# Optimization experiments

Hardware: AMD Instinct MI355X
Metric: run time of the kernel (lower is better)

## Reference

```python
import jax, jax.numpy as jnp
import numpy as np

N, T, D_IN, D_OUT = 131072, 16, 128, 128


def setup_inputs() -> dict:
    key = jax.random.key(0)
    k1, k2, k3, k4 = jax.random.split(key, 4)
    x = jax.random.normal(k1, (N, D_IN), dtype=jnp.float32)
    # sorted type ids, matching HeteroLinear(is_sorted=True)
    type_vec = jnp.sort(jax.random.randint(k2, (N,), 0, T)).astype(jnp.int32)
    # HeteroLinear weight: [num_types, in_channels, out_channels]; out = x @ W[t] + b[t]
    weight = (jax.random.normal(k3, (T, D_IN, D_OUT), dtype=jnp.float32)
              / np.float32(np.sqrt(D_IN)))
    bias = jax.random.normal(k4, (T, D_OUT), dtype=jnp.float32) * 0.01
    return {"x": x, "type_vec": type_vec, "weight": weight, "bias": bias}


def _grouped_matmul(x, weight, type_vec):
    """Segment (grouped) matmul: rows are sorted by type; row i uses weight[type_vec[i]]."""
    try:
        # Native grouped-GEMM primitive (exploits is_sorted=True contiguity).
        group_sizes = jnp.bincount(type_vec, length=weight.shape[0]).astype(jnp.int32)
        return jax.lax.ragged_dot(x, weight, group_sizes)
    except Exception:
        # Fallback: small fixed loop over the T types, masked accumulate.
        out = jnp.zeros((x.shape[0], weight.shape[-1]), dtype=x.dtype)
        for t in range(weight.shape[0]):
            out = out + jnp.where((type_vec == t)[:, None], x @ weight[t], jnp.zeros((), x.dtype))
        return out


def reference(x, type_vec, weight, bias):
    # ToHeteroLinear.fused_forward == HeteroLinear(x, type_vec):
    #   out[i] = x[i] @ weight[type_vec[i]] + bias[type_vec[i]]
    out = _grouped_matmul(x, weight, type_vec)  # [N, D_OUT]
    return out + bias[type_vec]
```

## Files before the change

### kernel.cpp

```cpp
#include <hip/hip_runtime.h>

#define DD 128
#define BM 64
#define CHUNK 2
#define T_TYPES 16

typedef __bf16 bf16x8 __attribute__((ext_vector_type(8)));
typedef float  f32x4  __attribute__((ext_vector_type(4)));

__device__ __forceinline__ void async_copy16(const void* g, void* l) {
    __builtin_amdgcn_global_load_lds(
        (const __attribute__((address_space(1))) unsigned int*)g,
        (__attribute__((address_space(3))) unsigned int*)l, 16, 0, 0);
}

__global__ __launch_bounds__(256) void transpose_w_frag_kernel(
    const float* __restrict__ w, unsigned short* __restrict__ wbf)
{
    __shared__ float lds[DD * 33];
    const int t   = blockIdx.x >> 2;
    const int n0  = (blockIdx.x & 3) * 32;
    const int tid = threadIdx.x;
    const float* wt = w + (size_t)t * DD * DD;

    #pragma unroll
    for (int i = 0; i < 4; ++i) {
        int f = tid + i * 256;
        int k = f >> 3;
        int c = (f & 7) * 4;
        float4 v = *(const float4*)&wt[k * DD + n0 + c];
        lds[k * 33 + c + 0] = v.x;
        lds[k * 33 + c + 1] = v.y;
        lds[k * 33 + c + 2] = v.z;
        lds[k * 33 + c + 3] = v.w;
    }
    __syncthreads();
    #pragma unroll
    for (int i = 0; i < 4; ++i) {
        int g  = tid + i * 256;
        int nl = g >> 5;
        int k4 = (g & 31) * 4;
        int n  = n0 + nl;
        int nt  = n >> 4, n16 = n & 15;
        int kk  = k4 >> 5, q = (k4 >> 3) & 3, jb = k4 & 7;
        int lane = q * 16 + n16;
        size_t ofs = ((((size_t)t * 8 + nt) * 4 + kk) * 64 + lane) * 8 + jb;
        ushort4 o;
        union { __bf16 b; unsigned short u; } cv;
        cv.b = (__bf16)lds[(k4 + 0) * 33 + nl]; o.x = cv.u;
        cv.b = (__bf16)lds[(k4 + 1) * 33 + nl]; o.y = cv.u;
        cv.b = (__bf16)lds[(k4 + 2) * 33 + nl]; o.z = cv.u;
        cv.b = (__bf16)lds[(k4 + 3) * 33 + nl]; o.w = cv.u;
        *(ushort4*)&wbf[ofs] = o;
    }
}

__global__ __launch_bounds__(256, 4) void hetero_main_kernel(
    const float* __restrict__ x,
    const int*   __restrict__ tv,
    const __bf16* __restrict__ wbf,
    const float* __restrict__ bias,
    float*       __restrict__ out)
{
    __shared__ __bf16 Bs[DD * DD];

    const int tid  = threadIdx.x;
    const int wave = tid >> 6;
    const int lane = tid & 63;
    const int q    = lane >> 4;
    const int n16  = lane & 15;
    const int chunk0 = blockIdx.x * (BM * CHUNK);

    int t_res = tv[chunk0];

    {
        const char* gsrc = (const char*)(wbf + (size_t)t_res * DD * DD);
        char* ldst = (char*)Bs;
        const int wofs = wave * 1024 + lane * 16;
        #pragma unroll
        for (int r = 0; r < 8; ++r)
            async_copy16(gsrc + r * 4096 + wofs, ldst + r * 4096 + wave * 1024);
    }

    float bv[8];
    #pragma unroll
    for (int nt = 0; nt < 8; ++nt) bv[nt] = bias[t_res * DD + nt * 16 + n16];

    f32x4 xlo[4], xhi[4];
    {
        const float* base = x + (size_t)(chunk0 + wave * 16 + n16) * DD + q * 8;
        #pragma unroll
        for (int kk = 0; kk < 4; ++kk) {
            xlo[kk] = *(const f32x4*)(base + kk * 32);
            xhi[kk] = *(const f32x4*)(base + kk * 32 + 4);
        }
    }

    __syncthreads();

    #pragma unroll
    for (int tile = 0; tile < CHUNK; ++tile) {
        const int trow0 = chunk0 + tile * BM;
        const int wrow0 = trow0 + wave * 16;

        f32x4 nlo[4], nhi[4];
        if (tile + 1 < CHUNK) {
            const float* base = x + (size_t)(wrow0 + BM + n16) * DD + q * 8;
            #pragma unroll
            for (int kk = 0; kk < 4; ++kk) {
                nlo[kk] = *(const f32x4*)(base + kk * 32);
                nhi[kk] = *(const f32x4*)(base + kk * 32 + 4);
            }
        }

        bf16x8 a[4];
        #pragma unroll
        for (int kk = 0; kk < 4; ++kk) {
            bf16x8 t;
            t[0] = (__bf16)xlo[kk][0]; t[1] = (__bf16)xlo[kk][1];
            t[2] = (__bf16)xlo[kk][2]; t[3] = (__bf16)xlo[kk][3];
            t[4] = (__bf16)xhi[kk][0]; t[5] = (__bf16)xhi[kk][1];
            t[6] = (__bf16)xhi[kk][2]; t[7] = (__bf16)xhi[kk][3];
            a[kk] = t;
        }

        const int tlo = tv[trow0];
        const int thi = tv[trow0 + BM - 1];

        for (int t = tlo; t <= thi; ++t) {
            if (t != t_res) {
                __syncthreads();
                const char* gsrc = (const char*)(wbf + (size_t)t * DD * DD);
                char* ldst = (char*)Bs;
                const int wofs = wave * 1024 + lane * 16;
                #pragma unroll
                for (int r = 0; r < 8; ++r)
                    async_copy16(gsrc + r * 4096 + wofs, ldst + r * 4096 + wave * 1024);
                t_res = t;
                #pragma unroll
                for (int nt = 0; nt < 8; ++nt) bv[nt] = bias[t * DD + nt * 16 + n16];
                __syncthreads();
            }

            f32x4 acc[8];
            #pragma unroll
            for (int nt = 0; nt < 8; ++nt) acc[nt] = (f32x4){0.f, 0.f, 0.f, 0.f};

            #pragma unroll
            for (int nt = 0; nt < 8; ++nt) {
                #pragma unroll
                for (int kk = 0; kk < 4; ++kk) {
                    bf16x8 b = *(const bf16x8*)&Bs[(((nt << 2) | kk) << 9) | (lane << 3)];
                    acc[nt] = __builtin_amdgcn_mfma_f32_16x16x32_bf16(a[kk], b, acc[nt], 0, 0, 0);
                }
            }

            const int rbase = wrow0 + q * 4;
            bool m0 = true, m1 = true, m2 = true, m3 = true;
            if (tlo != thi) {
                m0 = (tv[rbase + 0] == t);
                m1 = (tv[rbase + 1] == t);
                m2 = (tv[rbase + 2] == t);
                m3 = (tv[rbase + 3] == t);
            }
            float* o = out + (size_t)rbase * DD + n16;
            #pragma unroll
            for (int nt = 0; nt < 8; ++nt) {
                float* oc = o + nt * 16;
                if (m0) oc[0 * DD] = acc[nt][0] + bv[nt];
                if (m1) oc[1 * DD] = acc[nt][1] + bv[nt];
                if (m2) oc[2 * DD] = acc[nt][2] + bv[nt];
                if (m3) oc[3 * DD] = acc[nt][3] + bv[nt];
            }
        }

        #pragma unroll
        for (int kk = 0; kk < 4; ++kk) { xlo[kk] = nlo[kk]; xhi[kk] = nhi[kk]; }
    }
}

extern "C" void kernel_launch(void* const* d_in, const int* in_sizes, int n_in,
                              void* d_out, int out_size, void* d_ws, size_t ws_size,
                              hipStream_t stream) {
    const float* x    = (const float*)d_in[0];
    const int*   tv   = (const int*)d_in[1];
    const float* w    = (const float*)d_in[2];
    const float* bias = (const float*)d_in[3];
    float*       out  = (float*)d_out;
    unsigned short* wbf = (unsigned short*)d_ws;

    int nrows = in_sizes[0] / DD;
    int grid  = nrows / (BM * CHUNK);

    hipLaunchKernelGGL(transpose_w_frag_kernel, dim3(T_TYPES * 4), dim3(256), 0, stream,
                       w, wbf);
    hipLaunchKernelGGL(hetero_main_kernel, dim3(grid), dim3(256), 0, stream,
                       x, tv, (const __bf16*)wbf, bias, out);
}
```

Before: 123.2 us.

## Fuse weight bf16 conversion into main kernel, drop separate transpose pass

Removes the separate weight transpose/convert kernel and its workspace buffer. Each block now reads fp32 weights directly and converts them into the MFMA fragment layout in LDS with synchronous strided loads. This eliminates one kernel launch and the dependency between the two kernels. In exchange, every block repeats the conversion, reads twice as many weight bytes from L2, and gives up the async global-to-LDS copy.

```diff
diff --git a/kernel.cpp b/kernel.cpp
--- a/kernel.cpp
+++ b/kernel.cpp
@@ -8,57 +8,28 @@
 typedef __bf16 bf16x8 __attribute__((ext_vector_type(8)));
 typedef float  f32x4  __attribute__((ext_vector_type(4)));
 
-__device__ __forceinline__ void async_copy16(const void* g, void* l) {
-    __builtin_amdgcn_global_load_lds(
-        (const __attribute__((address_space(1))) unsigned int*)g,
-        (__attribute__((address_space(3))) unsigned int*)l, 16, 0, 0);
-}
-
-__global__ __launch_bounds__(256) void transpose_w_frag_kernel(
-    const float* __restrict__ w, unsigned short* __restrict__ wbf)
-{
-    __shared__ float lds[DD * 33];
-    const int t   = blockIdx.x >> 2;
-    const int n0  = (blockIdx.x & 3) * 32;
-    const int tid = threadIdx.x;
-    const float* wt = w + (size_t)t * DD * DD;
-
+__device__ __forceinline__ void build_B(const float* __restrict__ wt,
+                                        __bf16* __restrict__ Bs, int tid) {
     #pragma unroll
-    for (int i = 0; i < 4; ++i) {
-        int f = tid + i * 256;
-        int k = f >> 3;
-        int c = (f & 7) * 4;
-        float4 v = *(const float4*)&wt[k * DD + n0 + c];
-        lds[k * 33 + c + 0] = v.x;
-        lds[k * 33 + c + 1] = v.y;
-        lds[k * 33 + c + 2] = v.z;
-        lds[k * 33 + c + 3] = v.w;
-    }
-    __syncthreads();
-    #pragma unroll
-    for (int i = 0; i < 4; ++i) {
-        int g  = tid + i * 256;
-        int nl = g >> 5;
-        int k4 = (g & 31) * 4;
-        int n  = n0 + nl;
-        int nt  = n >> 4, n16 = n & 15;
-        int kk  = k4 >> 5, q = (k4 >> 3) & 3, jb = k4 & 7;
-        int lane = q * 16 + n16;
-        size_t ofs = ((((size_t)t * 8 + nt) * 4 + kk) * 64 + lane) * 8 + jb;
-        ushort4 o;
-        union { __bf16 b; unsigned short u; } cv;
-        cv.b = (__bf16)lds[(k4 + 0) * 33 + nl]; o.x = cv.u;
-        cv.b = (__bf16)lds[(k4 + 1) * 33 + nl]; o.y = cv.u;
-        cv.b = (__bf16)lds[(k4 + 2) * 33 + nl]; o.z = cv.u;
-        cv.b = (__bf16)lds[(k4 + 3) * 33 + nl]; o.w = cv.u;
-        *(ushort4*)&wbf[ofs] = o;
+    for (int i = 0; i < 8; ++i) {
+        int F    = tid + (i << 8);
+        int lane = F & 63;
+        int kk   = (F >> 6) & 3;
+        int nt   = F >> 8;
+        int q    = lane >> 4;
+        int n16  = lane & 15;
+        const float* p = wt + (kk * 32 + q * 8) * DD + nt * 16 + n16;
+        bf16x8 v;
+        #pragma unroll
+        for (int j = 0; j < 8; ++j) v[j] = (__bf16)p[j * DD];
+        *(bf16x8*)&Bs[(size_t)F * 8] = v;
     }
 }
 
-__global__ __launch_bounds__(256, 4) void hetero_main_kernel(
+__global__ __launch_bounds__(256, 4) void hetero_fused_kernel(
     const float* __restrict__ x,
     const int*   __restrict__ tv,
-    const __bf16* __restrict__ wbf,
+    const float* __restrict__ w,
     const float* __restrict__ bias,
     float*       __restrict__ out)
 {
@@ -73,19 +44,6 @@
 
     int t_res = tv[chunk0];
 
-    {
-        const char* gsrc = (const char*)(wbf + (size_t)t_res * DD * DD);
-        char* ldst = (char*)Bs;
-        const int wofs = wave * 1024 + lane * 16;
-        #pragma unroll
-        for (int r = 0; r < 8; ++r)
-            async_copy16(gsrc + r * 4096 + wofs, ldst + r * 4096 + wave * 1024);
-    }
-
-    float bv[8];
-    #pragma unroll
-    for (int nt = 0; nt < 8; ++nt) bv[nt] = bias[t_res * DD + nt * 16 + n16];
-
     f32x4 xlo[4], xhi[4];
     {
         const float* base = x + (size_t)(chunk0 + wave * 16 + n16) * DD + q * 8;
@@ -95,6 +53,12 @@
             xhi[kk] = *(const f32x4*)(base + kk * 32 + 4);
         }
     }
+
+    build_B(w + (size_t)t_res * DD * DD, Bs, tid);
+
+    float bv[8];
+    #pragma unroll
+    for (int nt = 0; nt < 8; ++nt) bv[nt] = bias[t_res * DD + nt * 16 + n16];
 
     __syncthreads();
 
@@ -130,12 +94,7 @@
         for (int t = tlo; t <= thi; ++t) {
             if (t != t_res) {
                 __syncthreads();
-                const char* gsrc = (const char*)(wbf + (size_t)t * DD * DD);
-                char* ldst = (char*)Bs;
-                const int wofs = wave * 1024 + lane * 16;
-                #pragma unroll
-                for (int r = 0; r < 8; ++r)
-                    async_copy16(gsrc + r * 4096 + wofs, ldst + r * 4096 + wave * 1024);
+                build_B(w + (size_t)t * DD * DD, Bs, tid);
                 t_res = t;
                 #pragma unroll
                 for (int nt = 0; nt < 8; ++nt) bv[nt] = bias[t * DD + nt * 16 + n16];
@@ -187,13 +146,10 @@
     const float* w    = (const float*)d_in[2];
     const float* bias = (const float*)d_in[3];
     float*       out  = (float*)d_out;
-    unsigned short* wbf = (unsigned short*)d_ws;
 
     int nrows = in_sizes[0] / DD;
     int grid  = nrows / (BM * CHUNK);
 
-    hipLaunchKernelGGL(transpose_w_frag_kernel, dim3(T_TYPES * 4), dim3(256), 0, stream,
-                       w, wbf);
-    hipLaunchKernelGGL(hetero_main_kernel, dim3(grid), dim3(256), 0, stream,
-                       x, tv, (const __bf16*)wbf, bias, out);
+    hipLaunchKernelGGL(hetero_fused_kernel, dim3(grid), dim3(256), 0, stream,
+                       x, tv, w, bias, out);
 }
```

After: 127.2 us. 3.3% more time.

## Process four row tiles per block with two-deep register prefetch of x

Applied to the files above, without the earlier changes.

Each block now covers four 64-row tiles instead of two, and keeps two tiles of x in registers so the load of tile i+2 is issued while tile i is computed. This deepens the global-load prefetch and spreads the per-block weight LDS fill over more rows. Occupancy is halved (launch bounds 4 to 2) and the grid halves, which adds register pressure and leaves fewer blocks to hide latency.

```diff
diff --git a/kernel.cpp b/kernel.cpp
--- a/kernel.cpp
+++ b/kernel.cpp
@@ -2,7 +2,7 @@
 
 #define DD 128
 #define BM 64
-#define CHUNK 2
+#define CHUNK 4
 #define T_TYPES 16
 
 typedef __bf16 bf16x8 __attribute__((ext_vector_type(8)));
@@ -55,7 +55,76 @@
     }
 }
 
-__global__ __launch_bounds__(256, 4) void hetero_main_kernel(
+#define PROCESS(XLO, XHI, TILE, PRE)                                          \
+  do {                                                                        \
+    const int trow0 = chunk0 + (TILE) * BM;                                   \
+    const int wrow0 = trow0 + wave * 16;                                      \
+    bf16x8 a[4];                                                              \
+    _Pragma("unroll")                                                         \
+    for (int kk = 0; kk < 4; ++kk) {                                          \
+      bf16x8 t8;                                                              \
+      t8[0] = (__bf16)XLO[kk][0]; t8[1] = (__bf16)XLO[kk][1];                 \
+      t8[2] = (__bf16)XLO[kk][2]; t8[3] = (__bf16)XLO[kk][3];                 \
+      t8[4] = (__bf16)XHI[kk][0]; t8[5] = (__bf16)XHI[kk][1];                 \
+      t8[6] = (__bf16)XHI[kk][2]; t8[7] = (__bf16)XHI[kk][3];                 \
+      a[kk] = t8;                                                             \
+    }                                                                         \
+    if (PRE) {            \
+      const float* bp = x + (size_t)(wrow0 + 2 * BM + n16) * DD + q * 8;      \
+      _Pragma("unroll")                                                       \
+      for (int kk = 0; kk < 4; ++kk) {                                        \
+        XLO[kk] = *(const f32x4*)(bp + kk * 32);                              \
+        XHI[kk] = *(const f32x4*)(bp + kk * 32 + 4);                          \
+      }                                                                       \
+    }                                                                         \
+    const int tlo = tv[trow0];                                                \
+    const int thi = tv[trow0 + BM - 1];                                       \
+    for (int t = tlo; t <= thi; ++t) {                                        \
+      if (t != t_res) {                       \
+        __syncthreads();                   \
+        const char* gsrc = (const char*)(wbf + (size_t)t * DD * DD);          \
+        char* ldst = (char*)Bs;                                               \
+        const int wofs = wave * 1024 + lane * 16;                             \
+        _Pragma("unroll")                                                     \
+        for (int r = 0; r < 8; ++r)                                           \
+          async_copy16(gsrc + r * 4096 + wofs, ldst + r * 4096 + wave * 1024);\
+        t_res = t;                                                            \
+        _Pragma("unroll")                                                     \
+        for (int nt = 0; nt < 8; ++nt) bv[nt] = bias[t * DD + nt * 16 + n16]; \
+        __syncthreads();                                                      \
+      }                                                                       \
+      f32x4 acc[8];                                                           \
+      _Pragma("unroll")                                                       \
+      for (int nt = 0; nt < 8; ++nt) acc[nt] = (f32x4){0.f, 0.f, 0.f, 0.f};   \
+      _Pragma("unroll")                                                       \
+      for (int nt = 0; nt < 8; ++nt) {                                        \
+        _Pragma("unroll")                                                     \
+        for (int kk = 0; kk < 4; ++kk) {                                      \
+          bf16x8 b = *(const bf16x8*)&Bs[(((nt << 2) | kk) << 9) | (lane << 3)];\
+          acc[nt] = __builtin_amdgcn_mfma_f32_16x16x32_bf16(a[kk], b, acc[nt], 0, 0, 0);\
+        }                                                                     \
+      }                                                                       \
+      const int rbase = wrow0 + q * 4;                                        \
+      bool m0 = true, m1 = true, m2 = true, m3 = true;                        \
+      if (tlo != thi) {                                                       \
+        m0 = (tv[rbase + 0] == t);                                            \
+        m1 = (tv[rbase + 1] == t);                                            \
+        m2 = (tv[rbase + 2] == t);                                            \
+        m3 = (tv[rbase + 3] == t);                                            \
+      }                                                                       \
+      float* o = out + (size_t)rbase * DD + n16;                              \
+      _Pragma("unroll")                                                       \
+      for (int nt = 0; nt < 8; ++nt) {                                        \
+        float* oc = o + nt * 16;                                              \
+        if (m0) oc[0 * DD] = acc[nt][0] + bv[nt];                             \
+        if (m1) oc[1 * DD] = acc[nt][1] + bv[nt];                             \
+        if (m2) oc[2 * DD] = acc[nt][2] + bv[nt];                             \
+        if (m3) oc[3 * DD] = acc[nt][3] + bv[nt];                             \
+      }                                                                       \
+    }                                                                         \
+  } while (0)
+
+__global__ __launch_bounds__(256, 2) void hetero_main_kernel(
     const float* __restrict__ x,
     const int*   __restrict__ tv,
     const __bf16* __restrict__ wbf,
@@ -86,97 +155,25 @@
     #pragma unroll
     for (int nt = 0; nt < 8; ++nt) bv[nt] = bias[t_res * DD + nt * 16 + n16];
 
-    f32x4 xlo[4], xhi[4];
+    f32x4 lo0[4], hi0[4], lo1[4], hi1[4];
     {
-        const float* base = x + (size_t)(chunk0 + wave * 16 + n16) * DD + q * 8;
+        const float* b0 = x + (size_t)(chunk0 + wave * 16 + n16) * DD + q * 8;
+        const float* b1 = b0 + (size_t)BM * DD;
         #pragma unroll
         for (int kk = 0; kk < 4; ++kk) {
-            xlo[kk] = *(const f32x4*)(base + kk * 32);
-            xhi[kk] = *(const f32x4*)(base + kk * 32 + 4);
+            lo0[kk] = *(const f32x4*)(b0 + kk * 32);
+            hi0[kk] = *(const f32x4*)(b0 + kk * 32 + 4);
+            lo1[kk] = *(const f32x4*)(b1 + kk * 32);
+            hi1[kk] = *(const f32x4*)(b1 + kk * 32 + 4);
         }
     }
 
     __syncthreads();
 
-    #pragma unroll
-    for (int tile = 0; tile < CHUNK; ++tile) {
-        const int trow0 = chunk0 + tile * BM;
-        const int wrow0 = trow0 + wave * 16;
-
-        f32x4 nlo[4], nhi[4];
-        if (tile + 1 < CHUNK) {
-            const float* base = x + (size_t)(wrow0 + BM + n16) * DD + q * 8;
-            #pragma unroll
-            for (int kk = 0; kk < 4; ++kk) {
-                nlo[kk] = *(const f32x4*)(base + kk * 32);
-                nhi[kk] = *(const f32x4*)(base + kk * 32 + 4);
-            }
-        }
-
-        bf16x8 a[4];
-        #pragma unroll
-        for (int kk = 0; kk < 4; ++kk) {
-            bf16x8 t;
-            t[0] = (__bf16)xlo[kk][0]; t[1] = (__bf16)xlo[kk][1];
-            t[2] = (__bf16)xlo[kk][2]; t[3] = (__bf16)xlo[kk][3];
-            t[4] = (__bf16)xhi[kk][0]; t[5] = (__bf16)xhi[kk][1];
-            t[6] = (__bf16)xhi[kk][2]; t[7] = (__bf16)xhi[kk][3];
-            a[kk] = t;
-        }
-
-        const int tlo = tv[trow0];
-        const int thi = tv[trow0 + BM - 1];
-
-        for (int t = tlo; t <= thi; ++t) {
-            if (t != t_res) {
-                __syncthreads();
-                const char* gsrc = (const char*)(wbf + (size_t)t * DD * DD);
-                char* ldst = (char*)Bs;
-                const int wofs = wave * 1024 + lane * 16;
-                #pragma unroll
-                for (int r = 0; r < 8; ++r)
-                    async_copy16(gsrc + r * 4096 + wofs, ldst + r * 4096 + wave * 1024);
-                t_res = t;
-                #pragma unroll
-                for (int nt = 0; nt < 8; ++nt) bv[nt] = bias[t * DD + nt * 16 + n16];
-                __syncthreads();
-            }
-
-            f32x4 acc[8];
-            #pragma unroll
-            for (int nt = 0; nt < 8; ++nt) acc[nt] = (f32x4){0.f, 0.f, 0.f, 0.f};
-
-            #pragma unroll
-            for (int nt = 0; nt < 8; ++nt) {
-                #pragma unroll
-                for (int kk = 0; kk < 4; ++kk) {
-                    bf16x8 b = *(const bf16x8*)&Bs[(((nt << 2) | kk) << 9) | (lane << 3)];
-                    acc[nt] = __builtin_amdgcn_mfma_f32_16x16x32_bf16(a[kk], b, acc[nt], 0, 0, 0);
-                }
-            }
-
-            const int rbase = wrow0 + q * 4;
-            bool m0 = true, m1 = true, m2 = true, m3 = true;
-            if (tlo != thi) {
-                m0 = (tv[rbase + 0] == t);
-                m1 = (tv[rbase + 1] == t);
-                m2 = (tv[rbase + 2] == t);
-                m3 = (tv[rbase + 3] == t);
-            }
-            float* o = out + (size_t)rbase * DD + n16;
-            #pragma unroll
-            for (int nt = 0; nt < 8; ++nt) {
-                float* oc = o + nt * 16;
-                if (m0) oc[0 * DD] = acc[nt][0] + bv[nt];
-                if (m1) oc[1 * DD] = acc[nt][1] + bv[nt];
-                if (m2) oc[2 * DD] = acc[nt][2] + bv[nt];
-                if (m3) oc[3 * DD] = acc[nt][3] + bv[nt];
-            }
-        }
-
-        #pragma unroll
-        for (int kk = 0; kk < 4; ++kk) { xlo[kk] = nlo[kk]; xhi[kk] = nhi[kk]; }
-    }
+    PROCESS(lo0, hi0, 0, true);
+    PROCESS(lo1, hi1, 1, true);
+    PROCESS(lo0, hi0, 2, false);
+    PROCESS(lo1, hi1, 3, false);
 }
 
 extern "C" void kernel_launch(void* const* d_in, const int* in_sizes, int n_in,
```

Result: no change. 124.6 us (+1.2%).
